# Optimization experiments

Hardware: AMD Instinct MI355X
Metric: run time of the kernel (lower is better)

Reference implementation:

```python
import jax, jax.numpy as jnp
import numpy as np

B, C, H, Wd = 4, 64, 64, 64
CP = C // 2


def setup_inputs() -> dict:
    key = jax.random.key(0)
    k1, k2, k3 = jax.random.split(key, 3)
    Fq_l = jax.random.normal(k1, (B, C, H, Wd), dtype=jnp.float32)
    Fp_l = jax.random.normal(k2, (B, C, H, Wd), dtype=jnp.float32)
    # 1x1 conv == linear over channel dim; weight [out_c, in_c]
    W = jax.random.normal(k3, (CP, C), dtype=jnp.float32) * (1.0 / np.sqrt(C))
    b = jnp.zeros((CP,), dtype=jnp.float32)
    return {"Fq_l": Fq_l, "Fp_l": Fp_l, "W": W, "b": b}


def reference(Fq_l, Fp_l, W, b):
    bsz, c, h, w = Fq_l.shape
    hw = h * w
    # shared 1x1 conv projection: [b, c, h, w] -> [b, c//2, hw]
    q = jnp.einsum('oc,bchw->bohw', W, Fq_l).reshape(bsz, -1, hw) + b[None, :, None]
    p = jnp.einsum('oc,bchw->bohw', W, Fp_l).reshape(bsz, -1, hw) + b[None, :, None]
    # similarity: [b, hw, hw]
    sim = jnp.einsum('bcn,bcm->bnm', q, p)
    attn = jax.nn.softmax(sim, axis=-1)
    # aligned: [b, hw, c] -> [b, c, h, w]
    v = Fp_l.reshape(bsz, c, hw)
    aligned = jnp.einsum('bnm,bcm->bnc', attn, v)
    return aligned.transpose(0, 2, 1).reshape(bsz, c, h, w)
```

## Files before the change

kernel.cpp:

```cpp
#include <hip/hip_runtime.h>

#define HW 4096
#define LOG2E 1.44269504088896340736f

typedef _Float16 half8  __attribute__((ext_vector_type(8)));
typedef __bf16   bf16x8 __attribute__((ext_vector_type(8)));
typedef float    f32x16 __attribute__((ext_vector_type(16)));
typedef float    f32x2  __attribute__((ext_vector_type(2)));

extern "C" __device__ float __ocml_native_exp2_f32(float);
static __device__ __forceinline__ float fexp2(float x) {
    return __ocml_native_exp2_f32(x);
}

static __device__ __forceinline__ unsigned cvtpk_bf16(float lo, float hi) {
    unsigned r;
    asm("v_cvt_pk_bf16_f32 %0, %1, %2" : "=v"(r) : "v"(lo), "v"(hi));
    return r;
}

static __device__ __forceinline__ f32x16 mfma16(uint4 a, uint4 b, f32x16 c) {
    return __builtin_amdgcn_mfma_f32_32x32x16_f16(
        __builtin_bit_cast(half8, a), __builtin_bit_cast(half8, b), c, 0, 0, 0);
}
static __device__ __forceinline__ f32x16 mfmab16(uint4 a, uint4 b, f32x16 c) {
    return __builtin_amdgcn_mfma_f32_32x32x16_bf16(
        __builtin_bit_cast(bf16x8, a), __builtin_bit_cast(bf16x8, b), c, 0, 0, 0);
}

__global__ __launch_bounds__(256) void prep_kernel(
    const float* __restrict__ Fq, const float* __restrict__ Fp,
    const float* __restrict__ W,  const float* __restrict__ bias,
    _Float16* __restrict__ q_ws, char* __restrict__ p_arr, char* __restrict__ v_arr)
{
    const int tid = threadIdx.x;
    const int b   = blockIdx.y;
    const int x   = blockIdx.x;

    if (x >= 64) {
        int mt = x - 64;
        int c5 = tid & 31, hi = (tid >> 5) & 1, chunk = (tid >> 6) & 1, chalf = tid >> 7;
        int c = chalf * 32 + c5;
        int m = mt * 32 + chunk * 16 + hi * 4;
        const float* src = Fp + ((size_t)(b * 64 + c) << 12) + m;
        float4 f0 = *(const float4*)src;
        float4 f1 = *(const float4*)(src + 8);
        uint4 o = make_uint4(cvtpk_bf16(f0.x, f0.y), cvtpk_bf16(f0.z, f0.w),
                             cvtpk_bf16(f1.x, f1.y), cvtpk_bf16(f1.z, f1.w));
        size_t tb = ((size_t)(((b * 128 + mt) * 2 + chalf) * 2 + chunk)) << 10;
        *(uint4*)(v_arr + tb + (size_t)((hi << 5) | c5) * 16) = o;
        return;
    }

    __shared__ float Wt[64][36];
    __shared__ float comb[128][33];

    for (int i = tid; i < 2048; i += 256)
        Wt[i & 63][i >> 6] = W[i];
    __syncthreads();

    const int isP   = x >> 5;
    const int nl    = tid & 127;
    const int chalf = tid >> 7;
    const int n     = ((x & 31) << 7) + nl;
    const float* in = (isP ? Fp : Fq) + (size_t)(b * 64 + chalf * 32) * HW + n;

    float acc[32];
    #pragma unroll
    for (int o = 0; o < 32; ++o) acc[o] = 0.f;

    for (int c = 0; c < 32; ++c) {
        float f = in[(size_t)c * HW];
        const float* wr = &Wt[chalf * 32 + c][0];
        #pragma unroll
        for (int o = 0; o < 32; o += 4) {
            float4 w4 = *(const float4*)(wr + o);
            acc[o]   += w4.x * f; acc[o+1] += w4.y * f;
            acc[o+2] += w4.z * f; acc[o+3] += w4.w * f;
        }
    }

    if (chalf) {
        #pragma unroll
        for (int o = 0; o < 32; ++o) comb[nl][o] = acc[o];
    }
    __syncthreads();
    if (chalf) return;

    #pragma unroll
    for (int o = 0; o < 32; ++o) acc[o] += comb[nl][o] + bias[o];

    if (!isP) {
        _Float16* dst = q_ws + ((size_t)(b * HW + n) << 5);
        #pragma unroll
        for (int g = 0; g < 4; ++g) {
            union { _Float16 h[8]; uint4 u; } pk;
            #pragma unroll
            for (int j = 0; j < 8; ++j) pk.h[j] = (_Float16)(acc[g * 8 + j] * LOG2E);
            *(uint4*)(dst + g * 8) = pk.u;
        }
    } else {
        int kt = n >> 5, ln = n & 31;
        #pragma unroll
        for (int chunk = 0; chunk < 2; ++chunk) {
            #pragma unroll
            for (int h2 = 0; h2 < 2; ++h2) {
                union { _Float16 h[8]; uint4 u; } pk;
                #pragma unroll
                for (int j = 0; j < 8; ++j) pk.h[j] = (_Float16)acc[chunk * 16 + h2 * 8 + j];
                size_t off = (((size_t)((b * 128 + kt) * 2 + chunk)) << 9) + (size_t)((h2 << 5) + ln) * 8;
                *(uint4*)(p_arr + off * 2) = pk.u;
            }
        }
    }
}

#define SOFTPART(S, A0, A1, LV) { \
    float e0=fexp2(S[0]),  e1=fexp2(S[1]),  e2=fexp2(S[2]),  e3=fexp2(S[3]); \
    float e4=fexp2(S[4]),  e5=fexp2(S[5]),  e6=fexp2(S[6]),  e7=fexp2(S[7]); \
    float e8=fexp2(S[8]),  e9=fexp2(S[9]),  e10=fexp2(S[10]), e11=fexp2(S[11]); \
    float e12=fexp2(S[12]), e13=fexp2(S[13]), e14=fexp2(S[14]), e15=fexp2(S[15]); \
    f32x2 t0 = (f32x2){e0,e1}   + (f32x2){e2,e3}; \
    f32x2 t1 = (f32x2){e4,e5}   + (f32x2){e6,e7}; \
    f32x2 t2 = (f32x2){e8,e9}   + (f32x2){e10,e11}; \
    f32x2 t3 = (f32x2){e12,e13} + (f32x2){e14,e15}; \
    LV += (t0 + t1) + (t2 + t3); \
    A0 = make_uint4(cvtpk_bf16(e0,e1),  cvtpk_bf16(e2,e3),  cvtpk_bf16(e4,e5),  cvtpk_bf16(e6,e7)); \
    A1 = make_uint4(cvtpk_bf16(e8,e9),  cvtpk_bf16(e10,e11), cvtpk_bf16(e12,e13), cvtpk_bf16(e14,e15)); \
}

#define TILE(P0,P1,V00,V01,V10,V11) { \
    f32x16 s0 = (f32x16)0.0f, s1 = (f32x16)0.0f; \
    s0 = mfma16(P0, q00, s0); s0 = mfma16(P1, q01, s0); \
    s1 = mfma16(P0, q10, s1); s1 = mfma16(P1, q11, s1); \
    uint4 A0, A1, B0, B1; \
    SOFTPART(s0, A0, A1, l0v) \
    SOFTPART(s1, B0, B1, l1v) \
    __builtin_amdgcn_s_setprio(1); \
    o00 = mfmab16(A0, V00, o00); o00 = mfmab16(A1, V01, o00); \
    o01 = mfmab16(A0, V10, o01); o01 = mfmab16(A1, V11, o01); \
    o10 = mfmab16(B0, V00, o10); o10 = mfmab16(B1, V01, o10); \
    o11 = mfmab16(B0, V10, o11); o11 = mfmab16(B1, V11, o11); \
    __builtin_amdgcn_s_setprio(0); \
}

__global__ __launch_bounds__(512, 2) void attn_kernel(
    const _Float16* __restrict__ q_ws, const char* __restrict__ p_arr,
    const char* __restrict__ v_arr, float* __restrict__ out)
{
    __shared__ float part[8][32][33];
    __shared__ float l_red[8][2][64];
    __shared__ float l_inv[64];

    const int tid  = threadIdx.x;
    const int lane = tid & 63;
    const int w    = tid >> 6;
    const int lo5  = lane & 31;
    const int hi   = lane >> 5;

    const int id   = blockIdx.x + (blockIdx.y << 6);
    const int b    = (id >> 1) & 3;
    const int qb   = (((id >> 3) << 1) | (id & 1)) << 6;

    uint4 q00, q01, q10, q11;
    {
        const _Float16* qp = q_ws + (((size_t)(b * HW) + qb + lo5) << 5) + (hi << 3);
        q00 = *(const uint4*)qp;
        q01 = *(const uint4*)(qp + 16);
        q10 = *(const uint4*)(qp + 1024);
        q11 = *(const uint4*)(qp + 1040);
    }

    const char* pb = p_arr + ((size_t)(b * 128 + w * 16) << 11) + (lane << 4);
    const char* vb = v_arr + ((size_t)(b * 128 + w * 16) << 12) + (lane << 4);

    f32x16 o00 = (f32x16)0.0f, o01 = (f32x16)0.0f, o10 = (f32x16)0.0f, o11 = (f32x16)0.0f;
    f32x2 l0v = (f32x2){0.f, 0.f}, l1v = (f32x2){0.f, 0.f};

    uint4 pA0, pA1, vA00, vA01, vA10, vA11;
    uint4 pB0, pB1, vB00, vB01, vB10, vB11;

#define LOADT(P0,P1,V00,V01,V10,V11,T) { \
    const char* pp = pb + ((size_t)(T) << 11); \
    P0 = *(const uint4*)pp; P1 = *(const uint4*)(pp + 1024); \
    const char* vp = vb + ((size_t)(T) << 12); \
    V00 = *(const uint4*)vp;          V01 = *(const uint4*)(vp + 1024); \
    V10 = *(const uint4*)(vp + 2048); V11 = *(const uint4*)(vp + 3072); }

    LOADT(pA0, pA1, vA00, vA01, vA10, vA11, 0)
    for (int i = 0; i < 8; ++i) {
        int t = 2 * i + 1;
        LOADT(pB0, pB1, vB00, vB01, vB10, vB11, t)
        TILE(pA0, pA1, vA00, vA01, vA10, vA11)
        int t2 = (t + 1 > 15) ? 15 : (t + 1);
        LOADT(pA0, pA1, vA00, vA01, vA10, vA11, t2)
        TILE(pB0, pB1, vB00, vB01, vB10, vB11)
    }

    l_red[w][0][lane] = l0v.x + l0v.y;
    l_red[w][1][lane] = l1v.x + l1v.y;
    __syncthreads();
    if (tid < 64) {
        int s_ = tid >> 5, qq = tid & 31;
        float sum = 0.f;
        #pragma unroll
        for (int w2 = 0; w2 < 8; ++w2)
            sum += l_red[w2][s_][qq] + l_red[w2][s_][qq + 32];
        l_inv[tid] = 1.0f / sum;
    }

#define EPIPASS(OC, S_, H_) { \
    __syncthreads(); \
    _Pragma("unroll") \
    for (int r = 0; r < 16; ++r) \
        part[w][(r & 3) + 8 * (r >> 2) + 4 * hi][lo5] = OC[r]; \
    __syncthreads(); \
    _Pragma("unroll") \
    for (int rep = 0; rep < 2; ++rep) { \
        int idx = rep * 512 + tid; \
        int c_ = idx >> 5, q_ = idx & 31; \
        float v_ = ((part[0][q_][c_] + part[1][q_][c_]) + (part[2][q_][c_] + part[3][q_][c_])) \
                 + ((part[4][q_][c_] + part[5][q_][c_]) + (part[6][q_][c_] + part[7][q_][c_])); \
        out[((size_t)(((b << 6) + ((H_) << 5) + c_)) << 12) + qb + ((S_) << 5) + q_] = v_ * l_inv[((S_) << 5) + q_]; \
    } \
}

    EPIPASS(o00, 0, 0)
    EPIPASS(o01, 0, 1)
    EPIPASS(o10, 1, 0)
    EPIPASS(o11, 1, 1)
}

extern "C" void kernel_launch(void* const* d_in, const int* in_sizes, int n_in,
                              void* d_out, int out_size, void* d_ws, size_t ws_size,
                              hipStream_t stream)
{
    const float* Fq = (const float*)d_in[0];
    const float* Fp = (const float*)d_in[1];
    const float* W  = (const float*)d_in[2];
    const float* bs = (const float*)d_in[3];
    float* out = (float*)d_out;

    _Float16* q_ws = (_Float16*)d_ws;
    char* p_arr = (char*)d_ws + (1 << 20);
    char* v_arr = (char*)d_ws + (2 << 20);

    prep_kernel<<<dim3(192, 4), 256, 0, stream>>>(Fq, Fp, W, bs, q_ws, p_arr, v_arr);
    attn_kernel<<<dim3(64, 4), 512, 0, stream>>>(q_ws, p_arr, v_arr, out);
}
```

Baseline: 30.22 us.

## Halve per-block query tile to 32 rows and double grid with higher occupancy

Each attention block now handles 32 query rows instead of 64, so the grid doubles from 256 to 512 blocks and launch bounds ask for 4 blocks per SM instead of 2. The double-buffered P/V register prefetch is replaced by a simple single-buffer load-then-compute loop. The aim is to fill more CUs and cut register pressure. The cost is that each P/V tile loaded from memory is reused for half as many queries, which doubles global/L2 traffic for P and V, and the explicit load/compute overlap is lost.

```diff
diff --git a/kernel.cpp b/kernel.cpp
--- a/kernel.cpp
+++ b/kernel.cpp
@@ -130,27 +130,23 @@
 }
 
 #define TILE(P0,P1,V00,V01,V10,V11) { \
-    f32x16 s0 = (f32x16)0.0f, s1 = (f32x16)0.0f; \
+    f32x16 s0 = (f32x16)0.0f; \
     s0 = mfma16(P0, q00, s0); s0 = mfma16(P1, q01, s0); \
-    s1 = mfma16(P0, q10, s1); s1 = mfma16(P1, q11, s1); \
-    uint4 A0, A1, B0, B1; \
+    uint4 A0, A1; \
     SOFTPART(s0, A0, A1, l0v) \
-    SOFTPART(s1, B0, B1, l1v) \
     __builtin_amdgcn_s_setprio(1); \
     o00 = mfmab16(A0, V00, o00); o00 = mfmab16(A1, V01, o00); \
     o01 = mfmab16(A0, V10, o01); o01 = mfmab16(A1, V11, o01); \
-    o10 = mfmab16(B0, V00, o10); o10 = mfmab16(B1, V01, o10); \
-    o11 = mfmab16(B0, V10, o11); o11 = mfmab16(B1, V11, o11); \
     __builtin_amdgcn_s_setprio(0); \
 }
 
-__global__ __launch_bounds__(512, 2) void attn_kernel(
+__global__ __launch_bounds__(512, 4) void attn_kernel(
     const _Float16* __restrict__ q_ws, const char* __restrict__ p_arr,
     const char* __restrict__ v_arr, float* __restrict__ out)
 {
     __shared__ float part[8][32][33];
-    __shared__ float l_red[8][2][64];
-    __shared__ float l_inv[64];
+    __shared__ float l_red[8][64];
+    __shared__ float l_inv[32];
 
     const int tid  = threadIdx.x;
     const int lane = tid & 63;
@@ -158,58 +154,48 @@
     const int lo5  = lane & 31;
     const int hi   = lane >> 5;
 
-    const int id   = blockIdx.x + (blockIdx.y << 6);
+    const int id   = blockIdx.x + (blockIdx.y << 7);
     const int b    = (id >> 1) & 3;
-    const int qb   = (((id >> 3) << 1) | (id & 1)) << 6;
-
-    uint4 q00, q01, q10, q11;
+    const int qb   = ((((id >> 3) << 1) | (id & 1))) << 5;
+
+    uint4 q00, q01;
     {
         const _Float16* qp = q_ws + (((size_t)(b * HW) + qb + lo5) << 5) + (hi << 3);
         q00 = *(const uint4*)qp;
         q01 = *(const uint4*)(qp + 16);
-        q10 = *(const uint4*)(qp + 1024);
-        q11 = *(const uint4*)(qp + 1040);
     }
 
     const char* pb = p_arr + ((size_t)(b * 128 + w * 16) << 11) + (lane << 4);
     const char* vb = v_arr + ((size_t)(b * 128 + w * 16) << 12) + (lane << 4);
 
-    f32x16 o00 = (f32x16)0.0f, o01 = (f32x16)0.0f, o10 = (f32x16)0.0f, o11 = (f32x16)0.0f;
-    f32x2 l0v = (f32x2){0.f, 0.f}, l1v = (f32x2){0.f, 0.f};
-
-    uint4 pA0, pA1, vA00, vA01, vA10, vA11;
-    uint4 pB0, pB1, vB00, vB01, vB10, vB11;
-
-#define LOADT(P0,P1,V00,V01,V10,V11,T) { \
+    f32x16 o00 = (f32x16)0.0f, o01 = (f32x16)0.0f;
+    f32x2 l0v = (f32x2){0.f, 0.f};
+
+    uint4 P0, P1, V00, V01, V10, V11;
+
+#define LOADT(T) { \
     const char* pp = pb + ((size_t)(T) << 11); \
     P0 = *(const uint4*)pp; P1 = *(const uint4*)(pp + 1024); \
     const char* vp = vb + ((size_t)(T) << 12); \
     V00 = *(const uint4*)vp;          V01 = *(const uint4*)(vp + 1024); \
     V10 = *(const uint4*)(vp + 2048); V11 = *(const uint4*)(vp + 3072); }
 
-    LOADT(pA0, pA1, vA00, vA01, vA10, vA11, 0)
-    for (int i = 0; i < 8; ++i) {
-        int t = 2 * i + 1;
-        LOADT(pB0, pB1, vB00, vB01, vB10, vB11, t)
-        TILE(pA0, pA1, vA00, vA01, vA10, vA11)
-        int t2 = (t + 1 > 15) ? 15 : (t + 1);
-        LOADT(pA0, pA1, vA00, vA01, vA10, vA11, t2)
-        TILE(pB0, pB1, vB00, vB01, vB10, vB11)
-    }
-
-    l_red[w][0][lane] = l0v.x + l0v.y;
-    l_red[w][1][lane] = l1v.x + l1v.y;
+    for (int t = 0; t < 16; ++t) {
+        LOADT(t)
+        TILE(P0, P1, V00, V01, V10, V11)
+    }
+
+    l_red[w][lane] = l0v.x + l0v.y;
     __syncthreads();
-    if (tid < 64) {
-        int s_ = tid >> 5, qq = tid & 31;
+    if (tid < 32) {
         float sum = 0.f;
         #pragma unroll
         for (int w2 = 0; w2 < 8; ++w2)
-            sum += l_red[w2][s_][qq] + l_red[w2][s_][qq + 32];
+            sum += l_red[w2][tid] + l_red[w2][tid + 32];
         l_inv[tid] = 1.0f / sum;
     }
 
-#define EPIPASS(OC, S_, H_) { \
+#define EPIPASS(OC, H_) { \
     __syncthreads(); \
     _Pragma("unroll") \
     for (int r = 0; r < 16; ++r) \
@@ -221,14 +207,12 @@
         int c_ = idx >> 5, q_ = idx & 31; \
         float v_ = ((part[0][q_][c_] + part[1][q_][c_]) + (part[2][q_][c_] + part[3][q_][c_])) \
                  + ((part[4][q_][c_] + part[5][q_][c_]) + (part[6][q_][c_] + part[7][q_][c_])); \
-        out[((size_t)(((b << 6) + ((H_) << 5) + c_)) << 12) + qb + ((S_) << 5) + q_] = v_ * l_inv[((S_) << 5) + q_]; \
+        out[((size_t)(((b << 6) + ((H_) << 5) + c_)) << 12) + qb + q_] = v_ * l_inv[q_]; \
     } \
 }
 
-    EPIPASS(o00, 0, 0)
-    EPIPASS(o01, 0, 1)
-    EPIPASS(o10, 1, 0)
-    EPIPASS(o11, 1, 1)
+    EPIPASS(o00, 0)
+    EPIPASS(o01, 1)
 }
 
 extern "C" void kernel_launch(void* const* d_in, const int* in_sizes, int n_in,
@@ -246,5 +230,5 @@
     char* v_arr = (char*)d_ws + (2 << 20);
 
     prep_kernel<<<dim3(192, 4), 256, 0, stream>>>(Fq, Fp, W, bs, q_ws, p_arr, v_arr);
-    attn_kernel<<<dim3(64, 4), 512, 0, stream>>>(q_ws, p_arr, v_arr, out);
-}
+    attn_kernel<<<dim3(128, 4), 512, 0, stream>>>(q_ws, p_arr, v_arr, out);
+}
```

Measured after the change: 33.28 us. +10.1%, slower.
